# Optimization experiments

Hardware: AMD Instinct MI355X
Metric: run time of the kernel (lower is better)

The kernel has to match this reference:

```python
import jax, jax.numpy as jnp
import numpy as np

B, L, C = 256, 168, 36   # batch, length, sensor channels
F = 64                   # number_filter
D = 256                  # token_d_model
DIV = 3                  # div_sa
STEP = L // DIV          # 56 chunks (L divisible by DIV)


def setup_inputs() -> dict:
    key = jax.random.key(0)
    ks = jax.random.split(key, 16)
    inp = {}
    inp["x"] = jax.random.normal(ks[0], (B, L, C), jnp.float32)
    # conv2d stack: kernel (5,1), padding same, with bias
    inp["w0"] = jax.random.normal(ks[1], (F, 1, 5, 1), jnp.float32) * (1.0 / np.sqrt(5))
    inp["b0"] = jnp.zeros((F,), jnp.float32)
    for i in range(1, 4):
        inp[f"w{i}"] = jax.random.normal(ks[1 + i], (F, F, 5, 1), jnp.float32) * (1.0 / np.sqrt(5 * F))
        inp[f"b{i}"] = jnp.zeros((F,), jnp.float32)
    # self-attention 1x1 conv1d projections (no bias): (F*DIV -> F)
    s = 1.0 / np.sqrt(DIV * F)
    inp["wq"] = jax.random.normal(ks[5], (F, DIV * F), jnp.float32) * s
    inp["wk"] = jax.random.normal(ks[6], (F, DIV * F), jnp.float32) * s
    inp["wv"] = jax.random.normal(ks[7], (F, DIV * F), jnp.float32) * s
    inp["wv1"] = jax.random.normal(ks[8], (F, DIV * F), jnp.float32) * s
    inp["gamma"] = jnp.zeros((1,), jnp.float32)
    # fc: Linear(F*C -> D)
    inp["fc_w"] = jax.random.normal(ks[9], (D, F * C), jnp.float32) * (1.0 / np.sqrt(F * C))
    inp["fc_b"] = jnp.zeros((D,), jnp.float32)
    return inp


def _conv2d_same(x, w, b):
    y = jax.lax.conv_general_dilated(
        x, w, window_strides=(1, 1), padding="SAME",
        dimension_numbers=("NCHW", "OIHW", "NCHW"))
    return y + b[None, :, None, None]


def reference(x, w0, b0, w1, b1, w2, b2, w3, b3, wq, wk, wv, wv1, gamma, fc_w, fc_b):
    h = x[:, None, :, :]  # (B,1,L,C)
    for w, b in ((w0, b0), (w1, b1), (w2, b2), (w3, b3)):
        h = jax.nn.relu(_conv2d_same(h, w, b))  # (B,F,L,C)
    # chunk the length dim into STEP blocks of DIV rows, flatten F-major: (B,STEP,F*DIV,C)
    xc = h.reshape(B, F, STEP, DIV, C).transpose(0, 2, 1, 3, 4).reshape(B, STEP, F * DIV, C)
    # 1x1 conv1d projections == matmul over the F*DIV axis
    f = jnp.einsum("qk,bskc->bsqc", wq, xc)    # (B,STEP,F,C)
    g = jnp.einsum("qk,bskc->bsqc", wk, xc)
    hv = jnp.einsum("qk,bskc->bsqc", wv, xc)
    v1 = jnp.einsum("qk,bskc->bsqc", wv1, xc)
    # scores[b,s,i,j] = sum_q f[...,i] g[...,j]; torch softmax(dim=1) of (B,C,C) -> axis i
    scores = jnp.einsum("bsqi,bsqj->bsij", f, g)  # (B,STEP,C,C)
    beta = jax.nn.softmax(scores, axis=2)
    o = gamma[0] * jnp.einsum("bsqi,bsij->bsqj", hv, beta) + v1  # (B,STEP,F,C)
    # cat chunks along last dim then permute(0,3,1,2) == (B,STEP,F,C) already
    o = jax.nn.relu(o).reshape(B, STEP, F * C)
    # dropout is identity in eval mode
    out = jax.nn.relu(o @ fc_w.T + fc_b)  # (B,STEP,D)
    return out
```

## Files before the change

### kernel.cpp

```cpp
#include <hip/hip_runtime.h>
#include <hip/hip_bf16.h>

#define BB   256
#define LL   168
#define CC   36
#define FF   64
#define SSTEP 56

typedef __attribute__((ext_vector_type(8))) _Float16 half8;
typedef __attribute__((ext_vector_type(4))) _Float16 half4;
typedef __attribute__((ext_vector_type(4))) float f32x4;
typedef __attribute__((ext_vector_type(4))) int i32x4;

#define MFMA16(a,b,c) __builtin_amdgcn_mfma_f32_16x16x32_f16(a,b,c,0,0,0)

__global__ __launch_bounds__(256) void k0_prep(
    const float* __restrict__ w1, const float* __restrict__ w2, const float* __restrict__ w3,
    const float* __restrict__ wq, const float* __restrict__ wk,
    const float* __restrict__ wv, const float* __restrict__ wv1,
    const float* __restrict__ fcw,
    _Float16* __restrict__ wcb, _Float16* __restrict__ pwb, _Float16* __restrict__ fcB)
{
    const int N1 = 61440;
    const int N2 = 49152;
    const int N3 = 589824;
    int idx = blockIdx.x * 256 + threadIdx.x;
    if (idx < N1) {
        int lin = idx;
        int j    = lin & 7;   lin >>= 3;
        int lane = lin & 63;  lin >>= 6;
        int mt   = lin & 3;   lin >>= 2;
        int t    = lin % 5;   lin /= 5;
        int kk   = lin & 1;
        int layer = lin >> 1;
        int fo = mt * 16 + (lane & 15);
        int fi = kk * 32 + (lane >> 4) * 8 + j;
        const float* w = (layer == 0) ? w1 : (layer == 1) ? w2 : w3;
        wcb[idx] = (_Float16)w[fo * 320 + fi * 5 + t];
    } else if (idx < N1 + N2) {
        int e = idx - N1;
        int p = e / 12288, r = e % 12288;
        int kkp = r / 2048, r2 = r % 2048;
        int wv_ = r2 / 512, r3 = r2 % 512;
        int lane = r3 / 8, j = r3 % 8;
        int q  = wv_ * 16 + (lane & 15);
        int kp = kkp * 32 + (lane >> 4) * 8 + j;
        int d  = kp >> 6, f = kp & 63;
        const float* w = (p == 0) ? wq : (p == 1) ? wk : (p == 2) ? wv : wv1;
        pwb[e] = (_Float16)w[q * 192 + f * 3 + d];
    } else if (idx < N1 + N2 + N3) {
        int e = idx - N1 - N2;
        int d = e / 2304, kc = e % 2304;
        int cc = kc >> 6, q = kc & 63;
        fcB[e] = (_Float16)fcw[d * 2304 + q * 36 + cc];
    }
}

__global__ __launch_bounds__(256, 4) void k1_conv_proj(
    const float* __restrict__ x,
    const float* __restrict__ w0, const float* __restrict__ cb0,
    const float* __restrict__ cb1, const float* __restrict__ cb2,
    const float* __restrict__ cb3,
    const _Float16* __restrict__ wcb,
    const _Float16* __restrict__ pwb,
    const float* __restrict__ gamma,
    _Float16* __restrict__ P,
    _Float16* __restrict__ O,
    int b_start)
{
    __shared__ int4 hbv[1440];
    __shared__ int4 obv[448];
    __shared__ float xl[176];
    char* hb  = (char*)hbv;
    char* ob  = (char*)obv;
    const int tid  = threadIdx.x;
    const int lane = tid & 63, wid = tid >> 6;
    const int c = blockIdx.x % CC, bl = blockIdx.x / CC, b = b_start + bl;
    const float gam = gamma[0];
    const int4 IZ = make_int4(0, 0, 0, 0);
    const f32x4 FZ = {0.f, 0.f, 0.f, 0.f};
    const int pfirst = (gam == 0.f) ? 3 : 0;

    if (tid < 16) hbv[tid] = IZ;
    if (tid >= 32 && tid < 112) hbv[1328 + tid] = IZ;
    if (tid < 176) {
        int l = tid - 2;
        xl[tid] = (l >= 0 && l < LL) ? x[((size_t)b * LL + l) * CC + c] : 0.f;
    }
    __syncthreads();

    {
        float wt0 = w0[lane*5], wt1 = w0[lane*5+1], wt2 = w0[lane*5+2],
              wt3 = w0[lane*5+3], wt4 = w0[lane*5+4];
        float bb = cb0[lane];
        const int l0 = wid * 42;
        float h0 = xl[l0], h1 = xl[l0+1], h2 = xl[l0+2], h3 = xl[l0+3];
        #pragma unroll 6
        for (int i = 0; i < 42; ++i) {
            float h4 = xl[l0 + i + 4];
            float a = bb + wt0*h0 + wt1*h1 + wt2*h2 + wt3*h3 + wt4*h4;
            int row = l0 + i + 2;
            *(_Float16*)(hb + row*128 + ((lane*2) ^ ((row&7)<<4))) = (_Float16)fmaxf(a, 0.f);
            h0 = h1; h1 = h2; h2 = h3; h3 = h4;
        }
    }
    __syncthreads();

    const int fo = lane & 15;
    const int g8 = (lane >> 4) << 4;

    #pragma unroll 1
    for (int layer = 0; layer < 3; ++layer) {
        const float* bias = (layer == 0) ? cb1 : (layer == 1) ? cb2 : cb3;
        f32x4 acc[4][3];
        #pragma unroll
        for (int mt = 0; mt < 4; ++mt)
            #pragma unroll
            for (int i = 0; i < 3; ++i) acc[mt][i] = FZ;

        #pragma unroll
        for (int kk = 0; kk < 2; ++kk) {
            const _Float16* wb = wcb + layer*20480 + kk*10240 + lane*8;
            const int cb = kk*64 + g8;
            #pragma unroll
            for (int t = 0; t < 5; ++t) {
                half8 a0 = *(const half8*)(wb + t*2048 + 0*512);
                half8 a1 = *(const half8*)(wb + t*2048 + 1*512);
                half8 a2 = *(const half8*)(wb + t*2048 + 2*512);
                half8 a3 = *(const half8*)(wb + t*2048 + 3*512);
                #pragma unroll
                for (int i = 0; i < 3; ++i) {
                    const int nt = wid + 4*i;
                    if (nt < 11) {
                        int row = nt*16 + fo + t;
                        half8 bf = *(const half8*)(hb + row*128 + (cb ^ ((row&7)<<4)));
                        acc[0][i] = MFMA16(a0, bf, acc[0][i]);
                        acc[1][i] = MFMA16(a1, bf, acc[1][i]);
                        acc[2][i] = MFMA16(a2, bf, acc[2][i]);
                        acc[3][i] = MFMA16(a3, bf, acc[3][i]);
                    }
                }
            }
        }
        __syncthreads();

        if (layer < 2) {
            #pragma unroll
            for (int mt = 0; mt < 4; ++mt) {
                const int fo0 = mt*16 + ((lane>>4)<<2);
                const float bb0 = bias[fo0], bb1 = bias[fo0+1],
                            bb2 = bias[fo0+2], bb3 = bias[fo0+3];
                #pragma unroll
                for (int i = 0; i < 3; ++i) {
                    const int nt = wid + 4*i;
                    const int l  = nt*16 + fo;
                    if (nt < 11 && l < LL) {
                        int row = l + 2;
                        half4 hv;
                        hv.x = (_Float16)fmaxf(acc[mt][i].x + bb0, 0.f);
                        hv.y = (_Float16)fmaxf(acc[mt][i].y + bb1, 0.f);
                        hv.z = (_Float16)fmaxf(acc[mt][i].z + bb2, 0.f);
                        hv.w = (_Float16)fmaxf(acc[mt][i].w + bb3, 0.f);
                        *(half4*)(hb + row*128 + ((fo0*2) ^ ((row&7)<<4))) = hv;
                    }
                }
            }
        } else {
            #pragma unroll
            for (int mt = 0; mt < 4; ++mt) {
                const int fo0 = mt*16 + ((lane>>4)<<2);
                const float bb0 = bias[fo0], bb1 = bias[fo0+1],
                            bb2 = bias[fo0+2], bb3 = bias[fo0+3];
                #pragma unroll
                for (int i = 0; i < 3; ++i) {
                    const int nt = wid + 4*i;
                    const int l  = nt*16 + fo;
                    if (nt < 11 && l < LL) {
                        const int s = l / 3, d = l - s*3;
                        const int ssw = (s & 7) << 4;
                        half4 hv;
                        hv.x = (_Float16)fmaxf(acc[mt][i].x + bb0, 0.f);
                        hv.y = (_Float16)fmaxf(acc[mt][i].y + bb1, 0.f);
                        hv.z = (_Float16)fmaxf(acc[mt][i].z + bb2, 0.f);
                        hv.w = (_Float16)fmaxf(acc[mt][i].w + bb3, 0.f);
                        *(half4*)(hb + s*384 + ((d*128 + fo0*2) ^ ssw)) = hv;
                    }
                }
            }
        }
        __syncthreads();
    }

    const half8 HZ = {(_Float16)0,(_Float16)0,(_Float16)0,(_Float16)0,
                      (_Float16)0,(_Float16)0,(_Float16)0,(_Float16)0};
    #pragma unroll 1
    for (int p = pfirst; p < 4; ++p) {
        f32x4 pacc[4] = {FZ, FZ, FZ, FZ};
        const _Float16* ab = pwb + p*12288 + wid*512 + lane*8;
        #pragma unroll
        for (int kkp = 0; kkp < 6; ++kkp) {
            half8 af = *(const half8*)(ab + kkp*2048);
            const int cb = kkp*64 + g8;
            #pragma unroll
            for (int nt = 0; nt < 4; ++nt) {
                const int s = nt*16 + fo;
                half8 bf = HZ;
                if (s < SSTEP)
                    bf = *(const half8*)(hb + s*384 + (cb ^ ((s&7)<<4)));
                pacc[nt] = MFMA16(af, bf, pacc[nt]);
            }
        }
        __syncthreads();
        const int q0 = wid*16 + ((lane>>4)<<2);
        const bool relu = (p == 3 && gam == 0.f);
        #pragma unroll
        for (int nt = 0; nt < 4; ++nt) {
            const int s = nt*16 + fo;
            if (s >= SSTEP) continue;
            half4 o;
            if (relu) {
                o.x = (_Float16)fmaxf(pacc[nt].x, 0.f);
                o.y = (_Float16)fmaxf(pacc[nt].y, 0.f);
                o.z = (_Float16)fmaxf(pacc[nt].z, 0.f);
                o.w = (_Float16)fmaxf(pacc[nt].w, 0.f);
            } else {
                o.x = (_Float16)pacc[nt].x;
                o.y = (_Float16)pacc[nt].y;
                o.z = (_Float16)pacc[nt].z;
                o.w = (_Float16)pacc[nt].w;
            }
            *(half4*)(ob + s*128 + ((q0*2) ^ ((s&7)<<4))) = o;
        }
        __syncthreads();
        for (int i = tid; i < 448; i += 256) {
            int s = i >> 3, j = i & 7;
            i32x4 v = *(const i32x4*)(ob + s*128 + ((j*16) ^ ((s&7)<<4)));
            const size_t bs = (size_t)bl * SSTEP + s;
            _Float16* dst = relu ? (O + bs*2304 + c*64 + j*8)
                                 : (P + (bs*4 + p)*2304 + c*64 + j*8);
            __builtin_nontemporal_store(v, (i32x4*)dst);
        }
    }
}

__global__ __launch_bounds__(256) void k2_attn(
    const _Float16* __restrict__ P,
    const float* __restrict__ gamma,
    _Float16* __restrict__ O)
{
    const float gam = gamma[0];
    if (gam == 0.f) return;
    const int bs  = blockIdx.x;
    const int tid = threadIdx.x;
    __shared__ float pb[4][CC][FF];
    __shared__ float sc[CC][CC];

    const size_t base = (size_t)bs * 4 * 2304;
    for (int idx = tid; idx < 4 * 2304; idx += 256)
        ((float*)pb)[idx] = (float)P[base + idx];
    __syncthreads();

    for (int idx = tid; idx < CC * CC; idx += 256) {
        int i = idx / CC, jj = idx % CC;
        float a = 0.f;
        for (int qq = 0; qq < FF; ++qq) a += pb[0][i][qq] * pb[1][jj][qq];
        sc[i][jj] = a;
    }
    __syncthreads();
    if (tid < CC) {
        int jj = tid;
        float m = -1e30f;
        for (int i = 0; i < CC; ++i) m = fmaxf(m, sc[i][jj]);
        float ssum = 0.f;
        for (int i = 0; i < CC; ++i) ssum += expf(sc[i][jj] - m);
        float inv = 1.f / ssum;
        for (int i = 0; i < CC; ++i) sc[i][jj] = expf(sc[i][jj] - m) * inv;
    }
    __syncthreads();

    for (int idx = tid; idx < FF * CC; idx += 256) {
        int qq = idx / CC, jj = idx % CC;
        float a = 0.f;
        for (int i = 0; i < CC; ++i) a += pb[2][i][qq] * sc[i][jj];
        float o = gam * a + pb[3][jj][qq];
        O[(size_t)bs * 2304 + jj * 64 + qq] = (_Float16)fmaxf(o, 0.f);
    }
}

__global__ __launch_bounds__(256) void k3_fc(
    const _Float16* __restrict__ O,
    const _Float16* __restrict__ fcB,
    const float* __restrict__ fcb,
    float* __restrict__ out,
    int rows, int gm)
{
    const int bm = blockIdx.x % gm, bn = blockIdx.x / gm;
    const int r0 = bm * 64, c0 = bn * 64;
    const int tid = threadIdx.x, lane = tid & 63, wid = tid >> 6;
    __shared__ _Float16 As[64][72];
    __shared__ _Float16 Bs[64][72];

    const f32x4 FZ = {0.f, 0.f, 0.f, 0.f};
    f32x4 acc[4] = {FZ, FZ, FZ, FZ};
    const int rr = tid >> 2, k8 = (tid & 3) * 8;
    const int4 IZ = make_int4(0, 0, 0, 0);
    const int fo = lane & 15, g = lane >> 4;

    for (int k0 = 0; k0 < 2304; k0 += 64) {
        __syncthreads();
        {
            const bool rok = (r0 + rr < rows);
            int4 a0 = rok ? *(const int4*)(O + (size_t)(r0 + rr) * 2304 + k0 + k8) : IZ;
            int4 a1 = rok ? *(const int4*)(O + (size_t)(r0 + rr) * 2304 + k0 + 32 + k8) : IZ;
            *(int4*)&As[rr][k8]      = a0;
            *(int4*)&As[rr][k8 + 32] = a1;
            *(int4*)&Bs[rr][k8]      = *(const int4*)(fcB + (size_t)(c0 + rr) * 2304 + k0 + k8);
            *(int4*)&Bs[rr][k8 + 32] = *(const int4*)(fcB + (size_t)(c0 + rr) * 2304 + k0 + 32 + k8);
        }
        __syncthreads();
        #pragma unroll
        for (int kk2 = 0; kk2 < 2; ++kk2) {
            const int ko = kk2*32 + g*8;
            half8 af = *(const half8*)&As[wid*16 + fo][ko];
            #pragma unroll
            for (int ct = 0; ct < 4; ++ct) {
                half8 bf = *(const half8*)&Bs[ct*16 + fo][ko];
                acc[ct] = MFMA16(af, bf, acc[ct]);
            }
        }
    }
    #pragma unroll
    for (int ct = 0; ct < 4; ++ct) {
        const int d = c0 + ct*16 + fo;
        const float bb = fcb[d];
        #pragma unroll
        for (int r = 0; r < 4; ++r) {
            const int row = r0 + wid*16 + g*4 + r;
            if (row < rows) out[(size_t)row * 256 + d] = fmaxf(acc[ct][r] + bb, 0.f);
        }
    }
}

extern "C" void kernel_launch(void* const* d_in, const int* in_sizes, int n_in,
                              void* d_out, int out_size, void* d_ws, size_t ws_size,
                              hipStream_t stream)
{
    const float* x     = (const float*)d_in[0];
    const float* w0    = (const float*)d_in[1];
    const float* b0    = (const float*)d_in[2];
    const float* w1    = (const float*)d_in[3];
    const float* b1    = (const float*)d_in[4];
    const float* w2    = (const float*)d_in[5];
    const float* b2    = (const float*)d_in[6];
    const float* w3    = (const float*)d_in[7];
    const float* b3    = (const float*)d_in[8];
    const float* wq    = (const float*)d_in[9];
    const float* wk    = (const float*)d_in[10];
    const float* wv    = (const float*)d_in[11];
    const float* wv1   = (const float*)d_in[12];
    const float* gamma = (const float*)d_in[13];
    const float* fcw   = (const float*)d_in[14];
    const float* fcb   = (const float*)d_in[15];
    float* out = (float*)d_out;

    const size_t fixedB = (size_t)(61440 + 49152 + 589824) * 2;
    const size_t perB   = (size_t)SSTEP * 4 * 2304 * 2 + (size_t)SSTEP * 2304 * 2;
    int Bc = 256;
    while (Bc > 1 && fixedB + (size_t)Bc * perB > ws_size) Bc >>= 1;

    char* ws = (char*)d_ws;
    _Float16* wcb = (_Float16*)ws;
    _Float16* pwb = wcb + 61440;
    _Float16* fcB = pwb + 49152;
    _Float16* P   = (_Float16*)(ws + fixedB);
    _Float16* O   = P + (size_t)Bc * SSTEP * 4 * 2304;

    const int prep_total = 61440 + 49152 + 589824;
    k0_prep<<<(prep_total + 255) / 256, 256, 0, stream>>>(w1, w2, w3, wq, wk, wv, wv1,
                                                          fcw, wcb, pwb, fcB);

    for (int bst = 0; bst < BB; bst += Bc) {
        int bcur = (bst + Bc <= BB) ? Bc : (BB - bst);
        k1_conv_proj<<<bcur * CC, 256, 0, stream>>>(x, w0, b0, b1, b2, b3,
                                                    wcb, pwb, gamma, P, O, bst);
        k2_attn<<<bcur * SSTEP, 256, 0, stream>>>(P, gamma, O);
        int rows = bcur * SSTEP;
        int gm = (rows + 63) / 64;
        k3_fc<<<gm * 4, 256, 0, stream>>>(O, fcB, fcb,
                                          out + (size_t)bst * SSTEP * 256, rows, gm);
    }
}
```

Measured before the change: 349.9 us.

## Process two channels per 512-thread conv block and run FC once over full batch

The conv/projection kernel now handles two sensor channels per block with 512 threads (two groups of four waves, each with its own LDS activation buffer). This halves the grid size and lets the output staging write 128 contiguous halves per sequence row, giving wider global stores. The O buffer is now sized for the full batch so the FC kernel runs once after all chunks instead of once per chunk. The block's LDS use roughly doubles, which may lower the number of resident blocks per CU.

```diff
diff --git a/kernel.cpp b/kernel.cpp
--- a/kernel.cpp
+++ b/kernel.cpp
@@ -56,7 +56,7 @@
     }
 }
 
-__global__ __launch_bounds__(256, 4) void k1_conv_proj(
+__global__ __launch_bounds__(512, 4) void k1_conv_proj(
     const float* __restrict__ x,
     const float* __restrict__ w0, const float* __restrict__ cb0,
     const float* __restrict__ cb1, const float* __restrict__ cb2,
@@ -68,39 +68,49 @@
     _Float16* __restrict__ O,
     int b_start)
 {
-    __shared__ int4 hbv[1440];
-    __shared__ int4 obv[448];
-    __shared__ float xl[176];
-    char* hb  = (char*)hbv;
+    __shared__ int4 hbv[2880];
+    __shared__ int4 obv[896];
+    __shared__ float xl[2][176];
     char* ob  = (char*)obv;
     const int tid  = threadIdx.x;
     const int lane = tid & 63, wid = tid >> 6;
-    const int c = blockIdx.x % CC, bl = blockIdx.x / CC, b = b_start + bl;
+    const int cw = wid >> 2;
+    const int wi = wid & 3;
+    const int cp = blockIdx.x % 18, bl = blockIdx.x / 18, b = b_start + bl;
+    const int c0 = cp * 2;
+    char* hbc = (char*)hbv + cw * 23040;
     const float gam = gamma[0];
     const int4 IZ = make_int4(0, 0, 0, 0);
     const f32x4 FZ = {0.f, 0.f, 0.f, 0.f};
     const int pfirst = (gam == 0.f) ? 3 : 0;
 
-    if (tid < 16) hbv[tid] = IZ;
-    if (tid >= 32 && tid < 112) hbv[1328 + tid] = IZ;
-    if (tid < 176) {
-        int l = tid - 2;
-        xl[tid] = (l >= 0 && l < LL) ? x[((size_t)b * LL + l) * CC + c] : 0.f;
+    if (tid < 32) hbv[(tid >> 4) * 1440 + (tid & 15)] = IZ;
+    if (tid >= 32 && tid < 192) {
+        int u = tid - 32;
+        hbv[(u / 80) * 1440 + 1360 + (u % 80)] = IZ;
+    }
+    if (tid < 352) {
+        int which = tid / 176, r = tid % 176;
+        int l = r - 2;
+        xl[which][r] = (l >= 0 && l < LL) ? x[((size_t)b * LL + l) * CC + c0 + which] : 0.f;
     }
     __syncthreads();
 
     {
+        const int cc = c0 + cw;
+        (void)cc;
         float wt0 = w0[lane*5], wt1 = w0[lane*5+1], wt2 = w0[lane*5+2],
               wt3 = w0[lane*5+3], wt4 = w0[lane*5+4];
         float bb = cb0[lane];
-        const int l0 = wid * 42;
-        float h0 = xl[l0], h1 = xl[l0+1], h2 = xl[l0+2], h3 = xl[l0+3];
+        const int l0 = wi * 42;
+        const float* xc = xl[cw];
+        float h0 = xc[l0], h1 = xc[l0+1], h2 = xc[l0+2], h3 = xc[l0+3];
         #pragma unroll 6
         for (int i = 0; i < 42; ++i) {
-            float h4 = xl[l0 + i + 4];
+            float h4 = xc[l0 + i + 4];
             float a = bb + wt0*h0 + wt1*h1 + wt2*h2 + wt3*h3 + wt4*h4;
             int row = l0 + i + 2;
-            *(_Float16*)(hb + row*128 + ((lane*2) ^ ((row&7)<<4))) = (_Float16)fmaxf(a, 0.f);
+            *(_Float16*)(hbc + row*128 + ((lane*2) ^ ((row&7)<<4))) = (_Float16)fmaxf(a, 0.f);
             h0 = h1; h1 = h2; h2 = h3; h3 = h4;
         }
     }
@@ -130,10 +140,10 @@
                 half8 a3 = *(const half8*)(wb + t*2048 + 3*512);
                 #pragma unroll
                 for (int i = 0; i < 3; ++i) {
-                    const int nt = wid + 4*i;
+                    const int nt = wi + 4*i;
                     if (nt < 11) {
                         int row = nt*16 + fo + t;
-                        half8 bf = *(const half8*)(hb + row*128 + (cb ^ ((row&7)<<4)));
+                        half8 bf = *(const half8*)(hbc + row*128 + (cb ^ ((row&7)<<4)));
                         acc[0][i] = MFMA16(a0, bf, acc[0][i]);
                         acc[1][i] = MFMA16(a1, bf, acc[1][i]);
                         acc[2][i] = MFMA16(a2, bf, acc[2][i]);
@@ -152,7 +162,7 @@
                             bb2 = bias[fo0+2], bb3 = bias[fo0+3];
                 #pragma unroll
                 for (int i = 0; i < 3; ++i) {
-                    const int nt = wid + 4*i;
+                    const int nt = wi + 4*i;
                     const int l  = nt*16 + fo;
                     if (nt < 11 && l < LL) {
                         int row = l + 2;
@@ -161,7 +171,7 @@
                         hv.y = (_Float16)fmaxf(acc[mt][i].y + bb1, 0.f);
                         hv.z = (_Float16)fmaxf(acc[mt][i].z + bb2, 0.f);
                         hv.w = (_Float16)fmaxf(acc[mt][i].w + bb3, 0.f);
-                        *(half4*)(hb + row*128 + ((fo0*2) ^ ((row&7)<<4))) = hv;
+                        *(half4*)(hbc + row*128 + ((fo0*2) ^ ((row&7)<<4))) = hv;
                     }
                 }
             }
@@ -173,7 +183,7 @@
                             bb2 = bias[fo0+2], bb3 = bias[fo0+3];
                 #pragma unroll
                 for (int i = 0; i < 3; ++i) {
-                    const int nt = wid + 4*i;
+                    const int nt = wi + 4*i;
                     const int l  = nt*16 + fo;
                     if (nt < 11 && l < LL) {
                         const int s = l / 3, d = l - s*3;
@@ -183,7 +193,7 @@
                         hv.y = (_Float16)fmaxf(acc[mt][i].y + bb1, 0.f);
                         hv.z = (_Float16)fmaxf(acc[mt][i].z + bb2, 0.f);
                         hv.w = (_Float16)fmaxf(acc[mt][i].w + bb3, 0.f);
-                        *(half4*)(hb + s*384 + ((d*128 + fo0*2) ^ ssw)) = hv;
+                        *(half4*)(hbc + s*384 + ((d*128 + fo0*2) ^ ssw)) = hv;
                     }
                 }
             }
@@ -196,7 +206,7 @@
     #pragma unroll 1
     for (int p = pfirst; p < 4; ++p) {
         f32x4 pacc[4] = {FZ, FZ, FZ, FZ};
-        const _Float16* ab = pwb + p*12288 + wid*512 + lane*8;
+        const _Float16* ab = pwb + p*12288 + wi*512 + lane*8;
         #pragma unroll
         for (int kkp = 0; kkp < 6; ++kkp) {
             half8 af = *(const half8*)(ab + kkp*2048);
@@ -206,12 +216,12 @@
                 const int s = nt*16 + fo;
                 half8 bf = HZ;
                 if (s < SSTEP)
-                    bf = *(const half8*)(hb + s*384 + (cb ^ ((s&7)<<4)));
+                    bf = *(const half8*)(hbc + s*384 + (cb ^ ((s&7)<<4)));
                 pacc[nt] = MFMA16(af, bf, pacc[nt]);
             }
         }
         __syncthreads();
-        const int q0 = wid*16 + ((lane>>4)<<2);
+        const int q0 = wi*16 + ((lane>>4)<<2);
         const bool relu = (p == 3 && gam == 0.f);
         #pragma unroll
         for (int nt = 0; nt < 4; ++nt) {
@@ -229,15 +239,21 @@
                 o.z = (_Float16)pacc[nt].z;
                 o.w = (_Float16)pacc[nt].w;
             }
-            *(half4*)(ob + s*128 + ((q0*2) ^ ((s&7)<<4))) = o;
-        }
-        __syncthreads();
-        for (int i = tid; i < 448; i += 256) {
-            int s = i >> 3, j = i & 7;
-            i32x4 v = *(const i32x4*)(ob + s*128 + ((j*16) ^ ((s&7)<<4)));
-            const size_t bs = (size_t)bl * SSTEP + s;
-            _Float16* dst = relu ? (O + bs*2304 + c*64 + j*8)
-                                 : (P + (bs*4 + p)*2304 + c*64 + j*8);
+            *(half4*)(ob + s*256 + cw*128 + ((q0*2) ^ ((s&7)<<4))) = o;
+        }
+        __syncthreads();
+        for (int i = tid; i < 896; i += 512) {
+            int s = i >> 4, j = i & 15;
+            int jh = j >> 3, jl = j & 7;
+            i32x4 v = *(const i32x4*)(ob + s*256 + jh*128 + ((jl*16) ^ ((s&7)<<4)));
+            _Float16* dst;
+            if (relu) {
+                const size_t bsO = (size_t)b * SSTEP + s;
+                dst = O + bsO*2304 + c0*64 + j*8;
+            } else {
+                const size_t bsP = (size_t)bl * SSTEP + s;
+                dst = P + (bsP*4 + p)*2304 + c0*64 + j*8;
+            }
             __builtin_nontemporal_store(v, (i32x4*)dst);
         }
     }
@@ -363,17 +379,18 @@
     const float* fcb   = (const float*)d_in[15];
     float* out = (float*)d_out;
 
-    const size_t fixedB = (size_t)(61440 + 49152 + 589824) * 2;
-    const size_t perB   = (size_t)SSTEP * 4 * 2304 * 2 + (size_t)SSTEP * 2304 * 2;
+    const size_t fixedB  = (size_t)(61440 + 49152 + 589824) * 2;
+    const size_t O_FULL  = (size_t)BB * SSTEP * 2304 * 2;
+    const size_t perB_P  = (size_t)SSTEP * 4 * 2304 * 2;
     int Bc = 256;
-    while (Bc > 1 && fixedB + (size_t)Bc * perB > ws_size) Bc >>= 1;
+    while (Bc > 1 && fixedB + O_FULL + (size_t)Bc * perB_P > ws_size) Bc >>= 1;
 
     char* ws = (char*)d_ws;
     _Float16* wcb = (_Float16*)ws;
     _Float16* pwb = wcb + 61440;
     _Float16* fcB = pwb + 49152;
-    _Float16* P   = (_Float16*)(ws + fixedB);
-    _Float16* O   = P + (size_t)Bc * SSTEP * 4 * 2304;
+    _Float16* O   = (_Float16*)(ws + fixedB);
+    _Float16* P   = O + (size_t)BB * SSTEP * 2304;
 
     const int prep_total = 61440 + 49152 + 589824;
     k0_prep<<<(prep_total + 255) / 256, 256, 0, stream>>>(w1, w2, w3, wq, wk, wv, wv1,
@@ -381,12 +398,10 @@
 
     for (int bst = 0; bst < BB; bst += Bc) {
         int bcur = (bst + Bc <= BB) ? Bc : (BB - bst);
-        k1_conv_proj<<<bcur * CC, 256, 0, stream>>>(x, w0, b0, b1, b2, b3,
+        k1_conv_proj<<<bcur * 18, 512, 0, stream>>>(x, w0, b0, b1, b2, b3,
                                                     wcb, pwb, gamma, P, O, bst);
-        k2_attn<<<bcur * SSTEP, 256, 0, stream>>>(P, gamma, O);
-        int rows = bcur * SSTEP;
-        int gm = (rows + 63) / 64;
-        k3_fc<<<gm * 4, 256, 0, stream>>>(O, fcB, fcb,
-                                          out + (size_t)bst * SSTEP * 256, rows, gm);
-    }
+        k2_attn<<<bcur * SSTEP, 256, 0, stream>>>(P, gamma,
+                                                  O + (size_t)bst * SSTEP * 2304);
+    }
+    k3_fc<<<224 * 4, 256, 0, stream>>>(O, fcB, fcb, out, BB * SSTEP, 224);
 }
```

Result: faster. 337.7 us (-3.5%).

## Use 512-thread blocks in conv/proj kernel and run FC once over full batch

Applied to the files above, without the earlier changes.

The conv+projection kernel now runs with 8 waves per block instead of 4, splitting the conv rows and projection output tiles across more waves so each wave holds fewer accumulators. The O buffer is sized for the whole batch so the final FC kernel is launched once after all chunks, not once per batch chunk. This aims to raise latency hiding and cut per-chunk launch overhead, but it uses more workspace and the tighter launch bound (512,6) may force register spills.

```diff
diff --git a/kernel.cpp b/kernel.cpp
--- a/kernel.cpp
+++ b/kernel.cpp
@@ -56,7 +56,7 @@
     }
 }
 
-__global__ __launch_bounds__(256, 4) void k1_conv_proj(
+__global__ __launch_bounds__(512, 6) void k1_conv_proj(
     const float* __restrict__ x,
     const float* __restrict__ w0, const float* __restrict__ cb0,
     const float* __restrict__ cb1, const float* __restrict__ cb2,
@@ -71,10 +71,10 @@
     __shared__ int4 hbv[1440];
     __shared__ int4 obv[448];
     __shared__ float xl[176];
-    char* hb  = (char*)hbv;
-    char* ob  = (char*)obv;
+    char* hb = (char*)hbv;
+    char* ob = (char*)obv;
     const int tid  = threadIdx.x;
-    const int lane = tid & 63, wid = tid >> 6;
+    const int lane = tid & 63, wi = tid >> 6;
     const int c = blockIdx.x % CC, bl = blockIdx.x / CC, b = b_start + bl;
     const float gam = gamma[0];
     const int4 IZ = make_int4(0, 0, 0, 0);
@@ -93,10 +93,10 @@
         float wt0 = w0[lane*5], wt1 = w0[lane*5+1], wt2 = w0[lane*5+2],
               wt3 = w0[lane*5+3], wt4 = w0[lane*5+4];
         float bb = cb0[lane];
-        const int l0 = wid * 42;
+        const int l0 = wi * 21;
         float h0 = xl[l0], h1 = xl[l0+1], h2 = xl[l0+2], h3 = xl[l0+3];
-        #pragma unroll 6
-        for (int i = 0; i < 42; ++i) {
+        #pragma unroll 7
+        for (int i = 0; i < 21; ++i) {
             float h4 = xl[l0 + i + 4];
             float a = bb + wt0*h0 + wt1*h1 + wt2*h2 + wt3*h3 + wt4*h4;
             int row = l0 + i + 2;
@@ -112,11 +112,11 @@
     #pragma unroll 1
     for (int layer = 0; layer < 3; ++layer) {
         const float* bias = (layer == 0) ? cb1 : (layer == 1) ? cb2 : cb3;
-        f32x4 acc[4][3];
+        f32x4 acc[4][2];
         #pragma unroll
         for (int mt = 0; mt < 4; ++mt)
             #pragma unroll
-            for (int i = 0; i < 3; ++i) acc[mt][i] = FZ;
+            for (int i = 0; i < 2; ++i) acc[mt][i] = FZ;
 
         #pragma unroll
         for (int kk = 0; kk < 2; ++kk) {
@@ -129,8 +129,8 @@
                 half8 a2 = *(const half8*)(wb + t*2048 + 2*512);
                 half8 a3 = *(const half8*)(wb + t*2048 + 3*512);
                 #pragma unroll
-                for (int i = 0; i < 3; ++i) {
-                    const int nt = wid + 4*i;
+                for (int i = 0; i < 2; ++i) {
+                    const int nt = wi + 8*i;
                     if (nt < 11) {
                         int row = nt*16 + fo + t;
                         half8 bf = *(const half8*)(hb + row*128 + (cb ^ ((row&7)<<4)));
@@ -151,8 +151,8 @@
                 const float bb0 = bias[fo0], bb1 = bias[fo0+1],
                             bb2 = bias[fo0+2], bb3 = bias[fo0+3];
                 #pragma unroll
-                for (int i = 0; i < 3; ++i) {
-                    const int nt = wid + 4*i;
+                for (int i = 0; i < 2; ++i) {
+                    const int nt = wi + 8*i;
                     const int l  = nt*16 + fo;
                     if (nt < 11 && l < LL) {
                         int row = l + 2;
@@ -172,8 +172,8 @@
                 const float bb0 = bias[fo0], bb1 = bias[fo0+1],
                             bb2 = bias[fo0+2], bb3 = bias[fo0+3];
                 #pragma unroll
-                for (int i = 0; i < 3; ++i) {
-                    const int nt = wid + 4*i;
+                for (int i = 0; i < 2; ++i) {
+                    const int nt = wi + 8*i;
                     const int l  = nt*16 + fo;
                     if (nt < 11 && l < LL) {
                         const int s = l / 3, d = l - s*3;
@@ -193,17 +193,19 @@
 
     const half8 HZ = {(_Float16)0,(_Float16)0,(_Float16)0,(_Float16)0,
                       (_Float16)0,(_Float16)0,(_Float16)0,(_Float16)0};
+    const int qs = wi & 3;
+    const int sh = wi >> 2;
     #pragma unroll 1
     for (int p = pfirst; p < 4; ++p) {
-        f32x4 pacc[4] = {FZ, FZ, FZ, FZ};
-        const _Float16* ab = pwb + p*12288 + wid*512 + lane*8;
+        f32x4 pacc[2] = {FZ, FZ};
+        const _Float16* ab = pwb + p*12288 + qs*512 + lane*8;
         #pragma unroll
         for (int kkp = 0; kkp < 6; ++kkp) {
             half8 af = *(const half8*)(ab + kkp*2048);
             const int cb = kkp*64 + g8;
             #pragma unroll
-            for (int nt = 0; nt < 4; ++nt) {
-                const int s = nt*16 + fo;
+            for (int nt = 0; nt < 2; ++nt) {
+                const int s = sh*32 + nt*16 + fo;
                 half8 bf = HZ;
                 if (s < SSTEP)
                     bf = *(const half8*)(hb + s*384 + (cb ^ ((s&7)<<4)));
@@ -211,11 +213,11 @@
             }
         }
         __syncthreads();
-        const int q0 = wid*16 + ((lane>>4)<<2);
+        const int q0 = qs*16 + ((lane>>4)<<2);
         const bool relu = (p == 3 && gam == 0.f);
         #pragma unroll
-        for (int nt = 0; nt < 4; ++nt) {
-            const int s = nt*16 + fo;
+        for (int nt = 0; nt < 2; ++nt) {
+            const int s = sh*32 + nt*16 + fo;
             if (s >= SSTEP) continue;
             half4 o;
             if (relu) {
@@ -232,12 +234,17 @@
             *(half4*)(ob + s*128 + ((q0*2) ^ ((s&7)<<4))) = o;
         }
         __syncthreads();
-        for (int i = tid; i < 448; i += 256) {
-            int s = i >> 3, j = i & 7;
+        if (tid < 448) {
+            int s = tid >> 3, j = tid & 7;
             i32x4 v = *(const i32x4*)(ob + s*128 + ((j*16) ^ ((s&7)<<4)));
-            const size_t bs = (size_t)bl * SSTEP + s;
-            _Float16* dst = relu ? (O + bs*2304 + c*64 + j*8)
-                                 : (P + (bs*4 + p)*2304 + c*64 + j*8);
+            _Float16* dst;
+            if (relu) {
+                const size_t bsO = (size_t)b * SSTEP + s;
+                dst = O + bsO*2304 + c*64 + j*8;
+            } else {
+                const size_t bsP = (size_t)bl * SSTEP + s;
+                dst = P + (bsP*4 + p)*2304 + c*64 + j*8;
+            }
             __builtin_nontemporal_store(v, (i32x4*)dst);
         }
     }
@@ -363,17 +370,18 @@
     const float* fcb   = (const float*)d_in[15];
     float* out = (float*)d_out;
 
-    const size_t fixedB = (size_t)(61440 + 49152 + 589824) * 2;
-    const size_t perB   = (size_t)SSTEP * 4 * 2304 * 2 + (size_t)SSTEP * 2304 * 2;
+    const size_t fixedB  = (size_t)(61440 + 49152 + 589824) * 2;
+    const size_t O_FULL  = (size_t)BB * SSTEP * 2304 * 2;
+    const size_t perB_P  = (size_t)SSTEP * 4 * 2304 * 2;
     int Bc = 256;
-    while (Bc > 1 && fixedB + (size_t)Bc * perB > ws_size) Bc >>= 1;
+    while (Bc > 1 && fixedB + O_FULL + (size_t)Bc * perB_P > ws_size) Bc >>= 1;
 
     char* ws = (char*)d_ws;
     _Float16* wcb = (_Float16*)ws;
     _Float16* pwb = wcb + 61440;
     _Float16* fcB = pwb + 49152;
-    _Float16* P   = (_Float16*)(ws + fixedB);
-    _Float16* O   = P + (size_t)Bc * SSTEP * 4 * 2304;
+    _Float16* O   = (_Float16*)(ws + fixedB);
+    _Float16* P   = O + (size_t)BB * SSTEP * 2304;
 
     const int prep_total = 61440 + 49152 + 589824;
     k0_prep<<<(prep_total + 255) / 256, 256, 0, stream>>>(w1, w2, w3, wq, wk, wv, wv1,
@@ -381,12 +389,10 @@
 
     for (int bst = 0; bst < BB; bst += Bc) {
         int bcur = (bst + Bc <= BB) ? Bc : (BB - bst);
-        k1_conv_proj<<<bcur * CC, 256, 0, stream>>>(x, w0, b0, b1, b2, b3,
+        k1_conv_proj<<<bcur * CC, 512, 0, stream>>>(x, w0, b0, b1, b2, b3,
                                                     wcb, pwb, gamma, P, O, bst);
-        k2_attn<<<bcur * SSTEP, 256, 0, stream>>>(P, gamma, O);
-        int rows = bcur * SSTEP;
-        int gm = (rows + 63) / 64;
-        k3_fc<<<gm * 4, 256, 0, stream>>>(O, fcB, fcb,
-                                          out + (size_t)bst * SSTEP * 256, rows, gm);
-    }
-}
+        k2_attn<<<bcur * SSTEP, 256, 0, stream>>>(P, gamma,
+                                                  O + (size_t)bst * SSTEP * 2304);
+    }
+    k3_fc<<<224 * 4, 256, 0, stream>>>(O, fcB, fcb, out, BB * SSTEP, 224);
+}
```

After: 502.4 us. +43.6%, slower.
